# Optimization experiments

Hardware: AMD Instinct MI355X
Metric: run time of the kernel (lower is better)

Reference implementation:

```python
import jax, jax.numpy as jnp
from jax import lax
import numpy as np

B, T, K = 256, 1024, 128


def setup_inputs() -> dict:
    key = jax.random.key(0)
    k1, k2, k3 = jax.random.split(key, 3)
    inputs = jax.random.normal(k1, (B, T, K), dtype=jnp.float32)
    transitions = jax.random.normal(k2, (K, K), dtype=jnp.float32)
    tags = jax.random.randint(k3, (B, T), 0, K, dtype=jnp.int64)
    mask = jnp.ones((B, T), dtype=jnp.int32)
    return {"inputs": inputs, "transitions": transitions, "tags": tags, "mask": mask}


def _input_likelihood(inputs, transitions, maskf):
    # inputs: [B,T,K] emissions; forward algorithm (no start/end transitions)
    emit = jnp.transpose(inputs, (1, 0, 2))  # [T,B,K]
    m = jnp.transpose(maskf, (1, 0))         # [T,B]
    alpha0 = emit[0]                          # [B,K]

    def step(alpha, xm):
        e, mi = xm  # e: [B,K], mi: [B]
        # inner[b,i,j] = alpha[b,i] + transitions[i,j] + e[b,j]
        inner = alpha[:, :, None] + transitions[None, :, :] + e[:, None, :]
        new = jax.nn.logsumexp(inner, axis=1)  # [B,K]
        alpha = new * mi[:, None] + alpha * (1.0 - mi[:, None])
        return alpha, None

    alpha, _ = lax.scan(step, alpha0, (emit[1:], m[1:]))
    return jax.nn.logsumexp(alpha, axis=-1)  # [B]


def _joint_likelihood(inputs, transitions, tags, mask, maskf):
    b, t, k = inputs.shape
    # transition scores between consecutive gold tags
    trans_scores = transitions[tags[:, :-1], tags[:, 1:]]              # [B,T-1]
    # emission scores at gold tags
    emit_scores = jnp.take_along_axis(inputs, tags[..., None], axis=2)[..., 0]  # [B,T]
    score = jnp.sum(trans_scores * maskf[:, 1:], axis=-1) \
          + jnp.sum(emit_scores[:, :-1] * maskf[:, :-1], axis=-1)
    # last valid tag's emission at the final timestep (AllenNLP semantics)
    last_idx = jnp.sum(mask, axis=1).astype(jnp.int32) - 1             # [B]
    last_tags = jnp.take_along_axis(tags, last_idx[:, None].astype(tags.dtype), axis=1)[:, 0]
    last_input_score = jnp.take_along_axis(inputs[:, -1, :], last_tags[:, None], axis=1)[:, 0]
    score = score + last_input_score * maskf[:, -1]
    return score  # [B]


def reference(inputs, transitions, tags, mask):
    maskf = mask.astype(inputs.dtype)
    log_denominator = _input_likelihood(inputs, transitions, maskf)
    log_numerator = _joint_likelihood(inputs, transitions, tags, mask, maskf)
    loglik = log_numerator - log_denominator
    return jnp.sum(loglik)  # reduction='sum'
```

## Files before the change

### kernel.cpp

```cpp
#include <hip/hip_runtime.h>
#include <math.h>

#define BB 256
#define TT 1024
#define KK 128
#define NB 16
#define NBLK (BB / NB)
#define NTHR 512
#define CHUNK 4
#define NCHUNK (TT / CHUNK)
#define PSTR 136

typedef __attribute__((ext_vector_type(8))) short bf16x8;
typedef __attribute__((ext_vector_type(4))) float f32x4;

__global__ void zero_out_kernel(float* out) { out[0] = 0.0f; }

__device__ __forceinline__ unsigned short f2bf(float x) {
    unsigned b = __float_as_uint(x);
    return (unsigned short)((b + 0x7FFFu + ((b >> 16) & 1u)) >> 16);
}

#define BARSYNC() { asm volatile("s_waitcnt lgkmcnt(0)" ::: "memory"); \
                    __builtin_amdgcn_s_barrier(); \
                    asm volatile("" ::: "memory"); }

__device__ __forceinline__ void ldb(const float* __restrict__ trans, int kbase, int jc,
                                    bf16x8& BH, bf16x8& BL) {
#pragma unroll
    for (int e = 0; e < 8; ++e) {
        float v = expf(trans[(size_t)(kbase + e) * KK + jc]);
        unsigned short hb = f2bf(v);
        float hv = __uint_as_float(((unsigned)hb) << 16);
        BH[e] = (short)hb;
        BL[e] = (short)f2bf(v - hv);
    }
}

__global__ __launch_bounds__(NTHR, 1) void crf_fwd(
    const float* __restrict__ inputs,
    const float* __restrict__ trans,
    const int* __restrict__ mask,
    float* __restrict__ out)
{
    __shared__ __align__(16) unsigned short pbuf[2][NB * PSTR];
    __shared__ __align__(16) float ebuf[2][CHUNK * NB * KK];
    __shared__ float mbuf[2][CHUNK * NB];

    const int tid = threadIdx.x;
    const int l   = tid & 63;
    const int w   = tid >> 6;
    const int r   = l & 15;
    const int kg  = l >> 4;
    const int jc  = w * 16 + (l & 15);
    const int j0  = w * 16 + kg * 4;
    const int b0  = blockIdx.x * NB;

    const int bb = tid >> 5;
    const int kq = tid & 31;
    const float* sbase = inputs + (size_t)(b0 + bb) * TT * KK + (size_t)kq * 4;
    const int xw = ((kq ^ bb) << 2);
    const int xg = (((w * 4 + kg) ^ r) << 2);

    bf16x8 Ah0, Ah1, Ah2, Ah3, Al0, Al1, Al2, Al3;
    ldb(trans,  0 + kg * 8, jc, Ah0, Al0);
    ldb(trans, 32 + kg * 8, jc, Ah1, Al1);
    ldb(trans, 64 + kg * 8, jc, Ah2, Al2);
    ldb(trans, 96 + kg * 8, jc, Ah3, Al3);

#pragma unroll
    for (int s = 0; s < CHUNK; ++s) {
        float4 e4 = *(const float4*)(sbase + (size_t)s * KK);
        e4.x = __expf(e4.x); e4.y = __expf(e4.y);
        e4.z = __expf(e4.z); e4.w = __expf(e4.w);
        *(float4*)&ebuf[0][(s * NB + bb) * KK + xw] = e4;
    }
    if (tid < CHUNK * NB) {
        int s = tid >> 4, bq = tid & 15;
        mbuf[0][s * NB + bq] = (float)mask[(size_t)(b0 + bq) * TT + s];
    }
    BARSYNC();

    float pcur0, pcur1, pcur2, pcur3;
    int m_int = 0;
    {
        float4 pc = *(const float4*)&ebuf[0][(0 * NB + r) * KK + xg];
        pcur0 = pc.x; pcur1 = pc.y; pcur2 = pc.z; pcur3 = pc.w;
        unsigned plo, phi;
        asm volatile("v_cvt_pk_bf16_f32 %0, %1, %2" : "=v"(plo) : "v"(pcur0), "v"(pcur1));
        asm volatile("v_cvt_pk_bf16_f32 %0, %1, %2" : "=v"(phi) : "v"(pcur2), "v"(pcur3));
        *(uint2*)&pbuf[0][r * PSTR + j0] = make_uint2(plo, phi);
    }
    BARSYNC();

#define STEP(S, RN) { \
    const unsigned short* Pp = pbuf[((S) + 1) & 1]; \
    unsigned short* Pn = pbuf[(S) & 1]; \
    float4 xv = *(const float4*)&eb[((S) * NB + r) * KK + xg]; \
    float mi = mb[(S) * NB + r]; \
    const unsigned short* pr = Pp + r * PSTR + kg * 8; \
    union { uint4 q; bf16x8 v; } a0, a1, a2, a3; \
    a0.q = *(const uint4*)(pr); \
    a1.q = *(const uint4*)(pr + 32); \
    a2.q = *(const uint4*)(pr + 64); \
    a3.q = *(const uint4*)(pr + 96); \
    f32x4 acch = {0.f, 0.f, 0.f, 0.f}; \
    f32x4 accl = {0.f, 0.f, 0.f, 0.f}; \
    acch = __builtin_amdgcn_mfma_f32_16x16x32_bf16(Ah0, a0.v, acch, 0, 0, 0); \
    accl = __builtin_amdgcn_mfma_f32_16x16x32_bf16(Al0, a0.v, accl, 0, 0, 0); \
    acch = __builtin_amdgcn_mfma_f32_16x16x32_bf16(Ah1, a1.v, acch, 0, 0, 0); \
    accl = __builtin_amdgcn_mfma_f32_16x16x32_bf16(Al1, a1.v, accl, 0, 0, 0); \
    acch = __builtin_amdgcn_mfma_f32_16x16x32_bf16(Ah2, a2.v, acch, 0, 0, 0); \
    accl = __builtin_amdgcn_mfma_f32_16x16x32_bf16(Al2, a2.v, accl, 0, 0, 0); \
    acch = __builtin_amdgcn_mfma_f32_16x16x32_bf16(Ah3, a3.v, acch, 0, 0, 0); \
    accl = __builtin_amdgcn_mfma_f32_16x16x32_bf16(Al3, a3.v, accl, 0, 0, 0); \
    float pn0 = (mi != 0.0f) ? (acch[0] + accl[0]) * xv.x : pcur0; \
    float pn1 = (mi != 0.0f) ? (acch[1] + accl[1]) * xv.y : pcur1; \
    float pn2 = (mi != 0.0f) ? (acch[2] + accl[2]) * xv.z : pcur2; \
    float pn3 = (mi != 0.0f) ? (acch[3] + accl[3]) * xv.w : pcur3; \
    if (RN) { \
        unsigned short u = Pp[r * PSTR]; \
        int Ex = (int)((u >> 7) & 255u) - 127; \
        float sc = __uint_as_float((unsigned)(127 - Ex) << 23); \
        pn0 *= sc; pn1 *= sc; pn2 *= sc; pn3 *= sc; \
        m_int += Ex; \
    } \
    pcur0 = pn0; pcur1 = pn1; pcur2 = pn2; pcur3 = pn3; \
    unsigned plo, phi; \
    asm volatile("v_cvt_pk_bf16_f32 %0, %1, %2" : "=v"(plo) : "v"(pn0), "v"(pn1)); \
    asm volatile("v_cvt_pk_bf16_f32 %0, %1, %2" : "=v"(phi) : "v"(pn2), "v"(pn3)); \
    *(uint2*)&Pn[r * PSTR + j0] = make_uint2(plo, phi); \
    BARSYNC(); }

    for (int c = 0; c < NCHUNK; ++c) {
        float4 pf0, pf1, pf2, pf3; int mpre = 0;
        if (c + 1 < NCHUNK) {
            const float* pb_ = sbase + (size_t)(c + 1) * CHUNK * KK;
            pf0 = *(const float4*)(pb_ + 0 * KK);
            pf1 = *(const float4*)(pb_ + 1 * KK);
            pf2 = *(const float4*)(pb_ + 2 * KK);
            pf3 = *(const float4*)(pb_ + 3 * KK);
            if (tid < CHUNK * NB)
                mpre = mask[(size_t)(b0 + (tid & 15)) * TT + (c + 1) * CHUNK + (tid >> 4)];
        }
        const float* eb = ebuf[c & 1];
        const float* mb = mbuf[c & 1];
        if (c == 0) {
            STEP(1, 0) STEP(2, 0) STEP(3, 1)
        } else {
            STEP(0, 0) STEP(1, 0) STEP(2, 0) STEP(3, 1)
        }
        if (c + 1 < NCHUNK) {
            float* en = ebuf[(c + 1) & 1];
            pf0.x = __expf(pf0.x); pf0.y = __expf(pf0.y); pf0.z = __expf(pf0.z); pf0.w = __expf(pf0.w);
            pf1.x = __expf(pf1.x); pf1.y = __expf(pf1.y); pf1.z = __expf(pf1.z); pf1.w = __expf(pf1.w);
            pf2.x = __expf(pf2.x); pf2.y = __expf(pf2.y); pf2.z = __expf(pf2.z); pf2.w = __expf(pf2.w);
            pf3.x = __expf(pf3.x); pf3.y = __expf(pf3.y); pf3.z = __expf(pf3.z); pf3.w = __expf(pf3.w);
            *(float4*)&en[(0 * NB + bb) * KK + xw] = pf0;
            *(float4*)&en[(1 * NB + bb) * KK + xw] = pf1;
            *(float4*)&en[(2 * NB + bb) * KK + xw] = pf2;
            *(float4*)&en[(3 * NB + bb) * KK + xw] = pf3;
            if (tid < CHUNK * NB)
                mbuf[(c + 1) & 1][(tid >> 4) * NB + (tid & 15)] = (float)mpre;
            BARSYNC();
        }
    }
#undef STEP

    float* aw = ebuf[0];
    {
        const float c2 = 0.69314718055994531f;
        float4 av;
        av.x = (float)m_int * c2 + logf(pcur0);
        av.y = (float)m_int * c2 + logf(pcur1);
        av.z = (float)m_int * c2 + logf(pcur2);
        av.w = (float)m_int * c2 + logf(pcur3);
        *(float4*)&aw[r * KK + j0] = av;
    }
    BARSYNC();
    {
        int bq = tid >> 5, l32 = tid & 31;
        const float* ab = aw + bq * KK;
        float4 av = *(const float4*)&ab[l32 * 4];
        float mx = fmaxf(fmaxf(av.x, av.y), fmaxf(av.z, av.w));
#pragma unroll
        for (int o = 1; o < 32; o <<= 1) mx = fmaxf(mx, __shfl_xor(mx, o));
        float ev = __expf(av.x - mx) + __expf(av.y - mx) + __expf(av.z - mx) + __expf(av.w - mx);
#pragma unroll
        for (int o = 1; o < 32; o <<= 1) ev += __shfl_xor(ev, o);
        if (l32 == 0) atomicAdd(out, -(mx + logf(ev)));
    }
}

__global__ __launch_bounds__(256, 1) void crf_num(
    const float* __restrict__ inputs,
    const float* __restrict__ trans,
    const int* __restrict__ tags,
    const int* __restrict__ mask,
    float* __restrict__ out)
{
    __shared__ float scratch[8];
    const int tid = threadIdx.x;
    const int b = blockIdx.x;
    const float* binp = inputs + (size_t)b * TT * KK;
    const int* bmask  = mask + (size_t)b * TT;
    const int* btags  = tags + (size_t)b * TT;
    float numpart = 0.0f, maskpart = 0.0f;
#pragma unroll
    for (int kk2 = 0; kk2 < TT / 256; ++kk2) {
        int t = tid + 256 * kk2;
        int tg = btags[t];
        float mf = (float)bmask[t];
        maskpart += mf;
        if (t < TT - 1) {
            int tg1   = btags[t + 1];
            float mf1 = (float)bmask[t + 1];
            numpart += trans[tg * KK + tg1] * mf1;
            numpart += binp[(size_t)t * KK + tg] * mf;
        }
    }
#pragma unroll
    for (int o = 1; o < 64; o <<= 1) numpart += __shfl_xor(numpart, o);
#pragma unroll
    for (int o = 1; o < 64; o <<= 1) maskpart += __shfl_xor(maskpart, o);
    if ((tid & 63) == 0) {
        scratch[tid >> 6]     = numpart;
        scratch[4 + (tid >> 6)] = maskpart;
    }
    __syncthreads();
    if (tid == 0) {
        float num  = (scratch[0] + scratch[1]) + (scratch[2] + scratch[3]);
        float msum = (scratch[4] + scratch[5]) + (scratch[6] + scratch[7]);
        int last_idx = (int)msum - 1;
        int ltag = btags[last_idx];
        num += binp[(size_t)(TT - 1) * KK + ltag] * (float)bmask[TT - 1];
        atomicAdd(out, num);
    }
}

extern "C" void kernel_launch(void* const* d_in, const int* in_sizes, int n_in,
                              void* d_out, int out_size, void* d_ws, size_t ws_size,
                              hipStream_t stream) {
    const float* inputs = (const float*)d_in[0];
    const float* trans  = (const float*)d_in[1];
    const int* tagsp    = (const int*)d_in[2];
    const int* maskp    = (const int*)d_in[3];
    float* out          = (float*)d_out;
    zero_out_kernel<<<1, 1, 0, stream>>>(out);
    crf_num<<<BB, 256, 0, stream>>>(inputs, trans, tagsp, maskp, out);
    crf_fwd<<<NBLK, NTHR, 0, stream>>>(inputs, trans, maskp, out);
}
```

Measured before the change: 743.0 us.

## Halve forward-kernel threads, each wave computes two 16-column tiles

The CRF forward kernel now runs 4 waves instead of 8 per block. Each wave holds transition fragments for two column tiles (j and j+64) and issues 16 MFMAs per step instead of 8, reusing the same loaded alpha fragments. The aim is to cut per-step barrier cost and LDS traffic for the serial recurrence, in exchange for more register pressure and a longer MFMA chain per wave. Emission prefetch and the final logsumexp reduction are reworked to match the 256-thread layout.

Result: slower. 908.5 us (+22.3%).

```diff
diff --git a/kernel.cpp b/kernel.cpp
--- a/kernel.cpp
+++ b/kernel.cpp
@@ -6,7 +6,7 @@
 #define KK 128
 #define NB 16
 #define NBLK (BB / NB)
-#define NTHR 512
+#define NTHR 256
 #define CHUNK 4
 #define NCHUNK (TT / CHUNK)
 #define PSTR 136
@@ -52,28 +52,48 @@
     const int w   = tid >> 6;
     const int r   = l & 15;
     const int kg  = l >> 4;
-    const int jc  = w * 16 + (l & 15);
-    const int j0  = w * 16 + kg * 4;
+    const int jca = w * 16 + (l & 15);
+    const int jcb = jca + 64;
+    const int j0a = w * 16 + kg * 4;
+    const int j0b = j0a + 64;
     const int b0  = blockIdx.x * NB;
 
-    const int bb = tid >> 5;
-    const int kq = tid & 31;
-    const float* sbase = inputs + (size_t)(b0 + bb) * TT * KK + (size_t)kq * 4;
-    const int xw = ((kq ^ bb) << 2);
-    const int xg = (((w * 4 + kg) ^ r) << 2);
-
-    bf16x8 Ah0, Ah1, Ah2, Ah3, Al0, Al1, Al2, Al3;
-    ldb(trans,  0 + kg * 8, jc, Ah0, Al0);
-    ldb(trans, 32 + kg * 8, jc, Ah1, Al1);
-    ldb(trans, 64 + kg * 8, jc, Ah2, Al2);
-    ldb(trans, 96 + kg * 8, jc, Ah3, Al3);
-
-#pragma unroll
-    for (int s = 0; s < CHUNK; ++s) {
-        float4 e4 = *(const float4*)(sbase + (size_t)s * KK);
-        e4.x = __expf(e4.x); e4.y = __expf(e4.y);
-        e4.z = __expf(e4.z); e4.w = __expf(e4.w);
-        *(float4*)&ebuf[0][(s * NB + bb) * KK + xw] = e4;
+    const int kq2 = tid & 31;
+    const int bbA = tid >> 5;
+    const int bbB = bbA + 8;
+    const float* gA = inputs + (size_t)(b0 + bbA) * TT * KK + (size_t)kq2 * 4;
+    const float* gB = inputs + (size_t)(b0 + bbB) * TT * KK + (size_t)kq2 * 4;
+    const int xwA = ((kq2 ^ bbA) << 2);
+    const int xwB = ((kq2 ^ bbB) << 2);
+    const int xga = (((w * 4 + kg) ^ r) << 2);
+
+    bf16x8 Aha0, Aha1, Aha2, Aha3, Ala0, Ala1, Ala2, Ala3;
+    bf16x8 Ahb0, Ahb1, Ahb2, Ahb3, Alb0, Alb1, Alb2, Alb3;
+    ldb(trans,  0 + kg * 8, jca, Aha0, Ala0);
+    ldb(trans, 32 + kg * 8, jca, Aha1, Ala1);
+    ldb(trans, 64 + kg * 8, jca, Aha2, Ala2);
+    ldb(trans, 96 + kg * 8, jca, Aha3, Ala3);
+    ldb(trans,  0 + kg * 8, jcb, Ahb0, Alb0);
+    ldb(trans, 32 + kg * 8, jcb, Ahb1, Alb1);
+    ldb(trans, 64 + kg * 8, jcb, Ahb2, Alb2);
+    ldb(trans, 96 + kg * 8, jcb, Ahb3, Alb3);
+
+#define XSTORE(DST, PF, I) { \
+    PF.x = __expf(PF.x); PF.y = __expf(PF.y); PF.z = __expf(PF.z); PF.w = __expf(PF.w); \
+    *(float4*)&DST[((((I) >> 1) * NB) + (((I) & 1) ? bbB : bbA)) * KK + (((I) & 1) ? xwB : xwA)] = PF; }
+
+    {
+        float4 p0 = *(const float4*)(gA + 0 * (size_t)KK);
+        float4 p1 = *(const float4*)(gB + 0 * (size_t)KK);
+        float4 p2 = *(const float4*)(gA + 1 * (size_t)KK);
+        float4 p3 = *(const float4*)(gB + 1 * (size_t)KK);
+        float4 p4 = *(const float4*)(gA + 2 * (size_t)KK);
+        float4 p5 = *(const float4*)(gB + 2 * (size_t)KK);
+        float4 p6 = *(const float4*)(gA + 3 * (size_t)KK);
+        float4 p7 = *(const float4*)(gB + 3 * (size_t)KK);
+        float* d0 = ebuf[0];
+        XSTORE(d0, p0, 0) XSTORE(d0, p1, 1) XSTORE(d0, p2, 2) XSTORE(d0, p3, 3)
+        XSTORE(d0, p4, 4) XSTORE(d0, p5, 5) XSTORE(d0, p6, 6) XSTORE(d0, p7, 7)
     }
     if (tid < CHUNK * NB) {
         int s = tid >> 4, bq = tid & 15;
@@ -81,22 +101,28 @@
     }
     BARSYNC();
 
-    float pcur0, pcur1, pcur2, pcur3;
+    float pa0, pa1, pa2, pa3, pb0, pb1, pb2, pb3;
     int m_int = 0;
     {
-        float4 pc = *(const float4*)&ebuf[0][(0 * NB + r) * KK + xg];
-        pcur0 = pc.x; pcur1 = pc.y; pcur2 = pc.z; pcur3 = pc.w;
-        unsigned plo, phi;
-        asm volatile("v_cvt_pk_bf16_f32 %0, %1, %2" : "=v"(plo) : "v"(pcur0), "v"(pcur1));
-        asm volatile("v_cvt_pk_bf16_f32 %0, %1, %2" : "=v"(phi) : "v"(pcur2), "v"(pcur3));
-        *(uint2*)&pbuf[0][r * PSTR + j0] = make_uint2(plo, phi);
+        float4 pca = *(const float4*)&ebuf[0][(0 * NB + r) * KK + xga];
+        float4 pcb = *(const float4*)&ebuf[0][(0 * NB + r) * KK + xga + 64];
+        pa0 = pca.x; pa1 = pca.y; pa2 = pca.z; pa3 = pca.w;
+        pb0 = pcb.x; pb1 = pcb.y; pb2 = pcb.z; pb3 = pcb.w;
+        unsigned ql, qh;
+        asm volatile("v_cvt_pk_bf16_f32 %0, %1, %2" : "=v"(ql) : "v"(pa0), "v"(pa1));
+        asm volatile("v_cvt_pk_bf16_f32 %0, %1, %2" : "=v"(qh) : "v"(pa2), "v"(pa3));
+        *(uint2*)&pbuf[0][r * PSTR + j0a] = make_uint2(ql, qh);
+        asm volatile("v_cvt_pk_bf16_f32 %0, %1, %2" : "=v"(ql) : "v"(pb0), "v"(pb1));
+        asm volatile("v_cvt_pk_bf16_f32 %0, %1, %2" : "=v"(qh) : "v"(pb2), "v"(pb3));
+        *(uint2*)&pbuf[0][r * PSTR + j0b] = make_uint2(ql, qh);
     }
     BARSYNC();
 
 #define STEP(S, RN) { \
     const unsigned short* Pp = pbuf[((S) + 1) & 1]; \
     unsigned short* Pn = pbuf[(S) & 1]; \
-    float4 xv = *(const float4*)&eb[((S) * NB + r) * KK + xg]; \
+    float4 xva = *(const float4*)&eb[((S) * NB + r) * KK + xga]; \
+    float4 xvb = *(const float4*)&eb[((S) * NB + r) * KK + xga + 64]; \
     float mi = mb[(S) * NB + r]; \
     const unsigned short* pr = Pp + r * PSTR + kg * 8; \
     union { uint4 q; bf16x8 v; } a0, a1, a2, a3; \
@@ -104,42 +130,65 @@
     a1.q = *(const uint4*)(pr + 32); \
     a2.q = *(const uint4*)(pr + 64); \
     a3.q = *(const uint4*)(pr + 96); \
-    f32x4 acch = {0.f, 0.f, 0.f, 0.f}; \
-    f32x4 accl = {0.f, 0.f, 0.f, 0.f}; \
-    acch = __builtin_amdgcn_mfma_f32_16x16x32_bf16(Ah0, a0.v, acch, 0, 0, 0); \
-    accl = __builtin_amdgcn_mfma_f32_16x16x32_bf16(Al0, a0.v, accl, 0, 0, 0); \
-    acch = __builtin_amdgcn_mfma_f32_16x16x32_bf16(Ah1, a1.v, acch, 0, 0, 0); \
-    accl = __builtin_amdgcn_mfma_f32_16x16x32_bf16(Al1, a1.v, accl, 0, 0, 0); \
-    acch = __builtin_amdgcn_mfma_f32_16x16x32_bf16(Ah2, a2.v, acch, 0, 0, 0); \
-    accl = __builtin_amdgcn_mfma_f32_16x16x32_bf16(Al2, a2.v, accl, 0, 0, 0); \
-    acch = __builtin_amdgcn_mfma_f32_16x16x32_bf16(Ah3, a3.v, acch, 0, 0, 0); \
-    accl = __builtin_amdgcn_mfma_f32_16x16x32_bf16(Al3, a3.v, accl, 0, 0, 0); \
-    float pn0 = (mi != 0.0f) ? (acch[0] + accl[0]) * xv.x : pcur0; \
-    float pn1 = (mi != 0.0f) ? (acch[1] + accl[1]) * xv.y : pcur1; \
-    float pn2 = (mi != 0.0f) ? (acch[2] + accl[2]) * xv.z : pcur2; \
-    float pn3 = (mi != 0.0f) ? (acch[3] + accl[3]) * xv.w : pcur3; \
+    f32x4 accha = {0.f, 0.f, 0.f, 0.f}; \
+    f32x4 accla = {0.f, 0.f, 0.f, 0.f}; \
+    f32x4 acchb = {0.f, 0.f, 0.f, 0.f}; \
+    f32x4 acclb = {0.f, 0.f, 0.f, 0.f}; \
+    accha = __builtin_amdgcn_mfma_f32_16x16x32_bf16(Aha0, a0.v, accha, 0, 0, 0); \
+    acchb = __builtin_amdgcn_mfma_f32_16x16x32_bf16(Ahb0, a0.v, acchb, 0, 0, 0); \
+    accla = __builtin_amdgcn_mfma_f32_16x16x32_bf16(Ala0, a0.v, accla, 0, 0, 0); \
+    acclb = __builtin_amdgcn_mfma_f32_16x16x32_bf16(Alb0, a0.v, acclb, 0, 0, 0); \
+    accha = __builtin_amdgcn_mfma_f32_16x16x32_bf16(Aha1, a1.v, accha, 0, 0, 0); \
+    acchb = __builtin_amdgcn_mfma_f32_16x16x32_bf16(Ahb1, a1.v, acchb, 0, 0, 0); \
+    accla = __builtin_amdgcn_mfma_f32_16x16x32_bf16(Ala1, a1.v, accla, 0, 0, 0); \
+    acclb = __builtin_amdgcn_mfma_f32_16x16x32_bf16(Alb1, a1.v, acclb, 0, 0, 0); \
+    accha = __builtin_amdgcn_mfma_f32_16x16x32_bf16(Aha2, a2.v, accha, 0, 0, 0); \
+    acchb = __builtin_amdgcn_mfma_f32_16x16x32_bf16(Ahb2, a2.v, acchb, 0, 0, 0); \
+    accla = __builtin_amdgcn_mfma_f32_16x16x32_bf16(Ala2, a2.v, accla, 0, 0, 0); \
+    acclb = __builtin_amdgcn_mfma_f32_16x16x32_bf16(Alb2, a2.v, acclb, 0, 0, 0); \
+    accha = __builtin_amdgcn_mfma_f32_16x16x32_bf16(Aha3, a3.v, accha, 0, 0, 0); \
+    acchb = __builtin_amdgcn_mfma_f32_16x16x32_bf16(Ahb3, a3.v, acchb, 0, 0, 0); \
+    accla = __builtin_amdgcn_mfma_f32_16x16x32_bf16(Ala3, a3.v, accla, 0, 0, 0); \
+    acclb = __builtin_amdgcn_mfma_f32_16x16x32_bf16(Alb3, a3.v, acclb, 0, 0, 0); \
+    float na0 = (mi != 0.0f) ? (accha[0] + accla[0]) * xva.x : pa0; \
+    float na1 = (mi != 0.0f) ? (accha[1] + accla[1]) * xva.y : pa1; \
+    float na2 = (mi != 0.0f) ? (accha[2] + accla[2]) * xva.z : pa2; \
+    float na3 = (mi != 0.0f) ? (accha[3] + accla[3]) * xva.w : pa3; \
+    float nb0 = (mi != 0.0f) ? (acchb[0] + acclb[0]) * xvb.x : pb0; \
+    float nb1 = (mi != 0.0f) ? (acchb[1] + acclb[1]) * xvb.y : pb1; \
+    float nb2 = (mi != 0.0f) ? (acchb[2] + acclb[2]) * xvb.z : pb2; \
+    float nb3 = (mi != 0.0f) ? (acchb[3] + acclb[3]) * xvb.w : pb3; \
     if (RN) { \
         unsigned short u = Pp[r * PSTR]; \
         int Ex = (int)((u >> 7) & 255u) - 127; \
         float sc = __uint_as_float((unsigned)(127 - Ex) << 23); \
-        pn0 *= sc; pn1 *= sc; pn2 *= sc; pn3 *= sc; \
+        na0 *= sc; na1 *= sc; na2 *= sc; na3 *= sc; \
+        nb0 *= sc; nb1 *= sc; nb2 *= sc; nb3 *= sc; \
         m_int += Ex; \
     } \
-    pcur0 = pn0; pcur1 = pn1; pcur2 = pn2; pcur3 = pn3; \
-    unsigned plo, phi; \
-    asm volatile("v_cvt_pk_bf16_f32 %0, %1, %2" : "=v"(plo) : "v"(pn0), "v"(pn1)); \
-    asm volatile("v_cvt_pk_bf16_f32 %0, %1, %2" : "=v"(phi) : "v"(pn2), "v"(pn3)); \
-    *(uint2*)&Pn[r * PSTR + j0] = make_uint2(plo, phi); \
+    pa0 = na0; pa1 = na1; pa2 = na2; pa3 = na3; \
+    pb0 = nb0; pb1 = nb1; pb2 = nb2; pb3 = nb3; \
+    unsigned ql, qh; \
+    asm volatile("v_cvt_pk_bf16_f32 %0, %1, %2" : "=v"(ql) : "v"(na0), "v"(na1)); \
+    asm volatile("v_cvt_pk_bf16_f32 %0, %1, %2" : "=v"(qh) : "v"(na2), "v"(na3)); \
+    *(uint2*)&Pn[r * PSTR + j0a] = make_uint2(ql, qh); \
+    asm volatile("v_cvt_pk_bf16_f32 %0, %1, %2" : "=v"(ql) : "v"(nb0), "v"(nb1)); \
+    asm volatile("v_cvt_pk_bf16_f32 %0, %1, %2" : "=v"(qh) : "v"(nb2), "v"(nb3)); \
+    *(uint2*)&Pn[r * PSTR + j0b] = make_uint2(ql, qh); \
     BARSYNC(); }
 
     for (int c = 0; c < NCHUNK; ++c) {
-        float4 pf0, pf1, pf2, pf3; int mpre = 0;
+        float4 pf0, pf1, pf2, pf3, pf4, pf5, pf6, pf7; int mpre = 0;
         if (c + 1 < NCHUNK) {
-            const float* pb_ = sbase + (size_t)(c + 1) * CHUNK * KK;
-            pf0 = *(const float4*)(pb_ + 0 * KK);
-            pf1 = *(const float4*)(pb_ + 1 * KK);
-            pf2 = *(const float4*)(pb_ + 2 * KK);
-            pf3 = *(const float4*)(pb_ + 3 * KK);
+            const size_t tb = (size_t)(c + 1) * CHUNK * KK;
+            pf0 = *(const float4*)(gA + tb + 0 * (size_t)KK);
+            pf1 = *(const float4*)(gB + tb + 0 * (size_t)KK);
+            pf2 = *(const float4*)(gA + tb + 1 * (size_t)KK);
+            pf3 = *(const float4*)(gB + tb + 1 * (size_t)KK);
+            pf4 = *(const float4*)(gA + tb + 2 * (size_t)KK);
+            pf5 = *(const float4*)(gB + tb + 2 * (size_t)KK);
+            pf6 = *(const float4*)(gA + tb + 3 * (size_t)KK);
+            pf7 = *(const float4*)(gB + tb + 3 * (size_t)KK);
             if (tid < CHUNK * NB)
                 mpre = mask[(size_t)(b0 + (tid & 15)) * TT + (c + 1) * CHUNK + (tid >> 4)];
         }
@@ -152,43 +201,46 @@
         }
         if (c + 1 < NCHUNK) {
             float* en = ebuf[(c + 1) & 1];
-            pf0.x = __expf(pf0.x); pf0.y = __expf(pf0.y); pf0.z = __expf(pf0.z); pf0.w = __expf(pf0.w);
-            pf1.x = __expf(pf1.x); pf1.y = __expf(pf1.y); pf1.z = __expf(pf1.z); pf1.w = __expf(pf1.w);
-            pf2.x = __expf(pf2.x); pf2.y = __expf(pf2.y); pf2.z = __expf(pf2.z); pf2.w = __expf(pf2.w);
-            pf3.x = __expf(pf3.x); pf3.y = __expf(pf3.y); pf3.z = __expf(pf3.z); pf3.w = __expf(pf3.w);
-            *(float4*)&en[(0 * NB + bb) * KK + xw] = pf0;
-            *(float4*)&en[(1 * NB + bb) * KK + xw] = pf1;
-            *(float4*)&en[(2 * NB + bb) * KK + xw] = pf2;
-            *(float4*)&en[(3 * NB + bb) * KK + xw] = pf3;
+            XSTORE(en, pf0, 0) XSTORE(en, pf1, 1) XSTORE(en, pf2, 2) XSTORE(en, pf3, 3)
+            XSTORE(en, pf4, 4) XSTORE(en, pf5, 5) XSTORE(en, pf6, 6) XSTORE(en, pf7, 7)
             if (tid < CHUNK * NB)
                 mbuf[(c + 1) & 1][(tid >> 4) * NB + (tid & 15)] = (float)mpre;
             BARSYNC();
         }
     }
 #undef STEP
+#undef XSTORE
 
     float* aw = ebuf[0];
     {
         const float c2 = 0.69314718055994531f;
         float4 av;
-        av.x = (float)m_int * c2 + logf(pcur0);
-        av.y = (float)m_int * c2 + logf(pcur1);
-        av.z = (float)m_int * c2 + logf(pcur2);
-        av.w = (float)m_int * c2 + logf(pcur3);
-        *(float4*)&aw[r * KK + j0] = av;
+        av.x = (float)m_int * c2 + logf(pa0);
+        av.y = (float)m_int * c2 + logf(pa1);
+        av.z = (float)m_int * c2 + logf(pa2);
+        av.w = (float)m_int * c2 + logf(pa3);
+        *(float4*)&aw[r * KK + j0a] = av;
+        av.x = (float)m_int * c2 + logf(pb0);
+        av.y = (float)m_int * c2 + logf(pb1);
+        av.z = (float)m_int * c2 + logf(pb2);
+        av.w = (float)m_int * c2 + logf(pb3);
+        *(float4*)&aw[r * KK + j0b] = av;
     }
     BARSYNC();
     {
-        int bq = tid >> 5, l32 = tid & 31;
+        int bq = tid >> 4, l16 = tid & 15;
         const float* ab = aw + bq * KK;
-        float4 av = *(const float4*)&ab[l32 * 4];
-        float mx = fmaxf(fmaxf(av.x, av.y), fmaxf(av.z, av.w));
-#pragma unroll
-        for (int o = 1; o < 32; o <<= 1) mx = fmaxf(mx, __shfl_xor(mx, o));
-        float ev = __expf(av.x - mx) + __expf(av.y - mx) + __expf(av.z - mx) + __expf(av.w - mx);
-#pragma unroll
-        for (int o = 1; o < 32; o <<= 1) ev += __shfl_xor(ev, o);
-        if (l32 == 0) atomicAdd(out, -(mx + logf(ev)));
+        float4 v1 = *(const float4*)&ab[l16 * 8];
+        float4 v2 = *(const float4*)&ab[l16 * 8 + 4];
+        float mx = fmaxf(fmaxf(fmaxf(v1.x, v1.y), fmaxf(v1.z, v1.w)),
+                         fmaxf(fmaxf(v2.x, v2.y), fmaxf(v2.z, v2.w)));
+#pragma unroll
+        for (int o = 1; o < 16; o <<= 1) mx = fmaxf(mx, __shfl_xor(mx, o));
+        float ev = __expf(v1.x - mx) + __expf(v1.y - mx) + __expf(v1.z - mx) + __expf(v1.w - mx)
+                 + __expf(v2.x - mx) + __expf(v2.y - mx) + __expf(v2.z - mx) + __expf(v2.w - mx);
+#pragma unroll
+        for (int o = 1; o < 16; o <<= 1) ev += __shfl_xor(ev, o);
+        if (l16 == 0) atomicAdd(out, -(mx + logf(ev)));
     }
 }
 
```
